# Optimization experiments

Hardware: AMD Instinct MI355X
Metric: run time of the kernel (lower is better)

Reference implementation:

```python
import jax, jax.numpy as jnp
import numpy as np

WL, FL = 64, 40
SCALE = 2.0 ** FL
CLIP_MAX = 2.0 ** (WL - FL - 1) - 2.0 ** (-FL)  # (2^(wl-1)-1)/2^fl
CLIP_MIN = -(2.0 ** (WL - FL - 1))
EPS = 1e-5
H = 8  # num_heads


def quant(x):
    # Fixed-point nearest-rounding quantizer: wl=64, fl=40.
    return jnp.clip(jnp.round(x * SCALE) / SCALE, CLIP_MIN, CLIP_MAX)


def setup_inputs() -> dict:
    key = jax.random.key(0)
    ks = jax.random.split(key, 9)
    N, S, C = 4096, 31, 512  # S = num_particles + 1 = 31 (hard-coded in module)
    SS = S * S
    return {
        "x": jax.random.normal(ks[0], (N, S, C), dtype=jnp.float32),
        "norm_gamma": jnp.ones((C,), jnp.float32),
        "norm_beta": jnp.zeros((C,), jnp.float32),
        "wq": jax.random.normal(ks[1], (C, C), jnp.float32) * 0.02,
        "wk": jax.random.normal(ks[2], (C, C), jnp.float32) * 0.02,
        "wv": jax.random.normal(ks[3], (C, C), jnp.float32) * 0.02,
        "wo": jax.random.normal(ks[4], (C, C), jnp.float32) * 0.02,
        "bo": jnp.zeros((C,), jnp.float32),
        "pre_gamma": jnp.ones((SS,), jnp.float32),
        "pre_beta": jnp.zeros((SS,), jnp.float32),
    }


def reference(x, norm_gamma, norm_beta, wq, wk, wv, wo, bo, pre_gamma, pre_beta):
    N, S, C = x.shape
    # BatchNorm1d(C) on x.transpose(1,2): per-channel stats over (batch, seq), training-mode (batch stats)
    mu = jnp.mean(x, axis=(0, 1))
    var = jnp.var(x, axis=(0, 1))
    out = quant((x - mu) * jax.lax.rsqrt(var + EPS) * norm_gamma + norm_beta)

    out_q = quant(out @ wq.T)
    out_k = quant(out @ wk.T)
    out_v = quant(out @ wv.T)

    q_ = out_q.reshape(N, S, H, C // H)
    k_ = out_k.reshape(N, S, H, C // H)
    v_ = out_v.reshape(N, S, H, C // H)

    energy = quant(jnp.einsum('nqhc,nkhc->nhqk', q_, k_))  # [N,H,S,S]

    # pre_exp_norm: BatchNorm1d(S*S) over reshaped energies; channel dim = S*S, stats over (batch, heads)
    e = energy.reshape(N, H, S * S)
    em = jnp.mean(e, axis=(0, 1))
    ev = jnp.var(e, axis=(0, 1))
    en = quant((e - em) * jax.lax.rsqrt(ev + EPS) * pre_gamma + pre_beta)
    energy_post = en.reshape(N, H, S, S)

    attention = quant(jax.nn.softmax(energy_post / jnp.sqrt(jnp.float32(C)), axis=-1))

    out = quant(jnp.einsum('nhql,nlhc->nqhc', attention, v_)).reshape(N, S, C)
    out = quant(out @ wo.T + bo)
    return quant(out + x)
```

## Files before the change

### kernel.cpp

```cpp
#include <hip/hip_runtime.h>
#include <cstdint>
#include <cstddef>

#define N_ 4096
#define S_ 31
#define C_ 512
#define H_ 8
#define M_ (N_*S_)
#define NH_ (N_*H_)

typedef unsigned short u16;
typedef unsigned char  u8;
typedef __bf16 v8bf __attribute__((ext_vector_type(8)));
typedef float  v4f  __attribute__((ext_vector_type(4)));
typedef float  v2f  __attribute__((ext_vector_type(2)));
typedef unsigned short v8u __attribute__((ext_vector_type(8)));

#define WS_STATS 2097152
#define WS_Q (WS_STATS + 32768)
#define WS_K (WS_Q + 67108864)
#define WS_V (WS_K + 67108864)

#define SCALE_QK 16.0f
#define SCALE_V  16.0f

__device__ __forceinline__ u16 f2bf(float f) {
  union { float f; unsigned u; } v; v.f = f;
  unsigned r = v.u + 0x7FFFu + ((v.u >> 16) & 1u);
  return (u16)(r >> 16);
}
__device__ __forceinline__ float bf2f(u16 v) {
  union { unsigned u; float f; } w; w.u = ((unsigned)v) << 16; return w.f;
}
__device__ __forceinline__ u8 enc1(float f) {
  return (u8)(__builtin_amdgcn_cvt_pk_fp8_f32(f, f, 0, false) & 0xff);
}
__device__ __forceinline__ unsigned enc4(float a, float b, float c, float d) {
  int w = __builtin_amdgcn_cvt_pk_fp8_f32(a, b, 0, false);
  w = __builtin_amdgcn_cvt_pk_fp8_f32(c, d, w, true);
  return (unsigned)w;
}
__device__ __forceinline__ v8bf dec8(uint2 u) {
  v2f p0 = __builtin_amdgcn_cvt_pk_f32_fp8((int)u.x, false);
  v2f p1 = __builtin_amdgcn_cvt_pk_f32_fp8((int)u.x, true);
  v2f p2 = __builtin_amdgcn_cvt_pk_f32_fp8((int)u.y, false);
  v2f p3 = __builtin_amdgcn_cvt_pk_f32_fp8((int)u.y, true);
  v8bf r;
  r[0]=(__bf16)p0[0]; r[1]=(__bf16)p0[1]; r[2]=(__bf16)p1[0]; r[3]=(__bf16)p1[1];
  r[4]=(__bf16)p2[0]; r[5]=(__bf16)p2[1]; r[6]=(__bf16)p3[0]; r[7]=(__bf16)p3[1];
  return r;
}

__global__ void k_init(const float* wq, const float* wk, const float* wv, const float* wo,
                       u16* wbf, float* statsf) {
  int gid = blockIdx.x * 256 + threadIdx.x;
  if (gid < 6144) statsf[gid] = 0.0f;
  int m = gid >> 18, o = gid & 262143;
  int e    = o & 7;
  int lane = (o >> 3) & 63;
  int kk   = (o >> 9) & 15;
  int j16  = o >> 13;
  int j = j16 * 16 + (lane & 15);
  int k = kk * 32 + (lane >> 4) * 8 + e;
  const float* src = (m == 0) ? wq : (m == 1) ? wk : (m == 2) ? wv : wo;
  wbf[(size_t)m * 262144 + o] = f2bf(src[j * 512 + k]);
}

__global__ void __launch_bounds__(512) k_xstats(const float* __restrict__ x, float* statsf) {
  int t = threadIdx.x;
  int c4 = (t & 127) * 4;
  int r0 = blockIdx.x * 512 + (t >> 7) * 128;
  float4 s = {0,0,0,0}, sq = {0,0,0,0};
  const float* p = x + (size_t)r0 * C_ + c4;
  for (int i = 0; i < 128; ++i) {
    float4 v = *(const float4*)(p + (size_t)i * C_);
    s.x += v.x; s.y += v.y; s.z += v.z; s.w += v.w;
    sq.x += v.x*v.x; sq.y += v.y*v.y; sq.z += v.z*v.z; sq.w += v.w*v.w;
  }
  atomicAdd(&statsf[c4+0], s.x); atomicAdd(&statsf[c4+1], s.y);
  atomicAdd(&statsf[c4+2], s.z); atomicAdd(&statsf[c4+3], s.w);
  atomicAdd(&statsf[512+c4+0], sq.x); atomicAdd(&statsf[512+c4+1], sq.y);
  atomicAdd(&statsf[512+c4+2], sq.z); atomicAdd(&statsf[512+c4+3], sq.w);
}

__global__ void k_finalize_ch(const float* gamma, const float* beta, float* statsf) {
  int c = threadIdx.x;
  float mu  = statsf[c] * (1.0f / (float)M_);
  float var = statsf[512 + c] * (1.0f / (float)M_) - mu * mu;
  float sc  = rsqrtf(var + 1e-5f) * gamma[c];
  statsf[1024 + c] = sc;
  statsf[1536 + c] = beta[c] - mu * sc;
}

__global__ void __launch_bounds__(512, 4)
k_qkv(const float* __restrict__ x, const u16* __restrict__ wbf,
      const float* __restrict__ statsf, u8* __restrict__ qg, u8* __restrict__ kg,
      u8* __restrict__ vt) {
  __shared__ float s_scale[C_], s_shift[C_];
  __shared__ u16 s_a[16*4*64*8];
  int t = threadIdx.x, nblk = blockIdx.x;
  int wave = t >> 6, lane = t & 63, l15 = lane & 15, quad = lane >> 4;
  s_scale[t] = statsf[1024+t]; s_shift[t] = statsf[1536+t];
  __syncthreads();

  const float* xb = x + (size_t)nblk * 2 * S_ * C_;
  for (int it = 0; it < 8; ++it) {
    int idx = t + it * 512;
    int row = idx >> 6, c8 = (idx & 63) << 3;
    int nl = row >> 5, s = row & 31;
    int kk = c8 >> 5, q4 = (c8 >> 3) & 3, mt = row >> 4, r15 = row & 15;
    u16* dst = s_a + ((((kk*4 + mt) << 6) | ((q4*16 + r15) ^ (kk & 7))) << 3);
    v8u o;
    if (s == 31) { o = (v8u){0,0,0,0,0,0,0,0}; }
    else {
      const float* g = xb + (size_t)(nl * 31 + s) * C_ + c8;
      float4 a = *(const float4*)g, b = *(const float4*)(g + 4);
      o[0]=f2bf(a.x*s_scale[c8+0]+s_shift[c8+0]); o[1]=f2bf(a.y*s_scale[c8+1]+s_shift[c8+1]);
      o[2]=f2bf(a.z*s_scale[c8+2]+s_shift[c8+2]); o[3]=f2bf(a.w*s_scale[c8+3]+s_shift[c8+3]);
      o[4]=f2bf(b.x*s_scale[c8+4]+s_shift[c8+4]); o[5]=f2bf(b.y*s_scale[c8+5]+s_shift[c8+5]);
      o[6]=f2bf(b.z*s_scale[c8+6]+s_shift[c8+6]); o[7]=f2bf(b.w*s_scale[c8+7]+s_shift[c8+7]);
    }
    *(v8u*)dst = o;
  }
  __syncthreads();

  #pragma unroll 1
  for (int ci = 0; ci < 3; ++ci) {
    const u16* B0 = wbf + (size_t)ci * 262144 + (size_t)wave * 32768 + (size_t)lane * 8;
    v4f acc[4][4];
    #pragma unroll
    for (int m = 0; m < 4; ++m)
      #pragma unroll
      for (int c = 0; c < 4; ++c) acc[m][c] = (v4f){0,0,0,0};

    #pragma unroll 2
    for (int kk = 0; kk < 16; ++kk) {
      v8bf a[4], b[4];
      #pragma unroll
      for (int m = 0; m < 4; ++m)
        a[m] = *(const v8bf*)(s_a + ((((kk*4 + m) << 6) | (lane ^ (kk & 7))) << 3));
      #pragma unroll
      for (int c = 0; c < 4; ++c)
        b[c] = *(const v8bf*)(B0 + (size_t)c * 8192 + kk * 512);
      #pragma unroll
      for (int m = 0; m < 4; ++m)
        #pragma unroll
        for (int c = 0; c < 4; ++c)
          acc[m][c] = __builtin_amdgcn_mfma_f32_16x16x32_bf16(a[m], b[c], acc[m][c], 0, 0, 0);
    }

    #pragma unroll
    for (int m = 0; m < 4; ++m) {
      int rbase = m*16 + quad*4;
      int nl = rbase >> 5, s0 = rbase & 31;
      size_t nbase = (size_t)(nblk*2 + nl) * 8;
      #pragma unroll
      for (int c = 0; c < 4; ++c) {
        int jj = wave*64 + c*16 + l15;
        int h = jj >> 6, d = jj & 63;
        if (ci == 2) {
          unsigned w = enc4(acc[m][c][0]*SCALE_V, acc[m][c][1]*SCALE_V,
                            acc[m][c][2]*SCALE_V, acc[m][c][3]*SCALE_V);
          *(unsigned*)(vt + ((nbase + h) * 2048) + d*32 + s0) = w;
        } else {
          u8* dst = ((ci == 0) ? qg : kg) + (nbase + h) * 2048 + (size_t)s0 * 64 + d;
          #pragma unroll
          for (int reg = 0; reg < 4; ++reg)
            dst[reg * 64] = enc1(acc[m][c][reg] * SCALE_QK);
        }
      }
    }
  }
}

__global__ void __launch_bounds__(512)
k_energy(u8* __restrict__ qg, const u8* __restrict__ kg) {
  int t = threadIdx.x;
  int wave = t >> 6, lane = t & 63, l15 = lane & 15, quad = lane >> 4;
  size_t nh = (size_t)blockIdx.x * 8 + wave;
  const u8* qp = qg + nh * 2048;
  const u8* kp = kg + nh * 2048;
  v8bf A[2][2], B[2][2];
  #pragma unroll
  for (int mt = 0; mt < 2; ++mt)
    #pragma unroll
    for (int kk = 0; kk < 2; ++kk) {
      A[mt][kk] = dec8(*(const uint2*)(qp + (mt*16 + l15)*64 + kk*32 + quad*8));
      B[mt][kk] = dec8(*(const uint2*)(kp + (mt*16 + l15)*64 + kk*32 + quad*8));
    }
  v4f acc[2][2];
  #pragma unroll
  for (int qt = 0; qt < 2; ++qt)
    #pragma unroll
    for (int kt = 0; kt < 2; ++kt) {
      v4f a = {0,0,0,0};
      a = __builtin_amdgcn_mfma_f32_16x16x32_bf16(A[qt][0], B[kt][0], a, 0, 0, 0);
      a = __builtin_amdgcn_mfma_f32_16x16x32_bf16(A[qt][1], B[kt][1], a, 0, 0, 0);
      acc[qt][kt] = a;
    }
  u16* ep = (u16*)(qg + nh * 2048);
  const float inv = 1.0f / (SCALE_QK * SCALE_QK);
  #pragma unroll
  for (int qt = 0; qt < 2; ++qt)
    #pragma unroll
    for (int kt = 0; kt < 2; ++kt) {
      int k = kt*16 + l15;
      #pragma unroll
      for (int reg = 0; reg < 4; ++reg) {
        int q = qt*16 + quad*4 + reg;
        ep[q*32 + k] = f2bf(acc[qt][kt][reg] * inv);
      }
    }
}

__global__ void __launch_bounds__(256) k_estats(const u16* __restrict__ eg, float* statsf) {
  int t = threadIdx.x;
  int r0 = blockIdx.x * 128;
  float s[4] = {0,0,0,0}, sq[4] = {0,0,0,0};
  for (int i = 0; i < 128; ++i) {
    uint2 u = *(const uint2*)(eg + (size_t)(r0 + i) * 1024 + t * 4);
    float v0 = bf2f((u16)(u.x & 0xffff)), v1 = bf2f((u16)(u.x >> 16));
    float v2 = bf2f((u16)(u.y & 0xffff)), v3 = bf2f((u16)(u.y >> 16));
    s[0]+=v0; s[1]+=v1; s[2]+=v2; s[3]+=v3;
    sq[0]+=v0*v0; sq[1]+=v1*v1; sq[2]+=v2*v2; sq[3]+=v3*v3;
  }
  #pragma unroll
  for (int j = 0; j < 4; ++j) {
    atomicAdd(&statsf[2048 + t*4 + j], s[j]);
    atomicAdd(&statsf[3072 + t*4 + j], sq[j]);
  }
}

__global__ void k_finalize_e(const float* pg, const float* pb, float* statsf) {
  int c = threadIdx.x;
  int q = c >> 5, k = c & 31;
  const float invC = 0.04419417382415922f;
  float s2 = 0.f, sh2 = 0.f;
  if (q < 31 && k < 31) {
    int ss = q*31 + k;
    float mu  = statsf[2048 + c] * (1.0f / (float)NH_);
    float var = statsf[3072 + c] * (1.0f / (float)NH_) - mu * mu;
    float sc  = rsqrtf(var + 1e-5f) * pg[ss];
    s2  = sc * invC;
    sh2 = (pb[ss] - mu * sc) * invC;
  }
  statsf[4096 + c] = s2;
  statsf[5120 + c] = sh2;
}

__global__ void __launch_bounds__(512, 4)
k_oproj(const float* __restrict__ x, const u16* __restrict__ wbf,
        const float* __restrict__ statsf, const u16* __restrict__ eg,
        const u8* __restrict__ vt, const float* __restrict__ bo, float* __restrict__ out) {
  __shared__ u16 s_a[16*4*64*8];
  __shared__ u16 s_attn[8][1024];
  int t = threadIdx.x, nblk = blockIdx.x;
  int wave = t >> 6, lane = t & 63, l15 = lane & 15, quad = lane >> 4;

  int q = lane & 31, half = lane >> 5;
  #pragma unroll 1
  for (int tk = 0; tk < 2; ++tk) {
    int task = wave * 2 + tk;
    int nl = task >> 3, h = task & 7;
    size_t nh = (size_t)(nblk*2 + nl) * 8 + h;
    const u16* ep = eg + nh * 1024;
    int cb = q*32 + half*16;
    v8u e0 = *(const v8u*)(ep + cb);
    v8u e1 = *(const v8u*)(ep + cb + 8);
    const float* s2g  = statsf + 4096 + cb;
    const float* sh2g = statsf + 5120 + cb;
    float lg[16];
    #pragma unroll
    for (int j = 0; j < 8; ++j) lg[j]   = bf2f(e0[j]) * s2g[j]   + sh2g[j];
    #pragma unroll
    for (int j = 0; j < 8; ++j) lg[8+j] = bf2f(e1[j]) * s2g[8+j] + sh2g[8+j];
    if (half) lg[15] = -1e30f;
    float mx = lg[0];
    #pragma unroll
    for (int j = 1; j < 16; ++j) mx = fmaxf(mx, lg[j]);
    mx = fmaxf(mx, __shfl_xor(mx, 32));
    float sum = 0.f;
    #pragma unroll
    for (int j = 0; j < 16; ++j) { lg[j] = __expf(lg[j] - mx); sum += lg[j]; }
    sum += __shfl_xor(sum, 32);
    float r = (q == 31) ? 0.f : (1.0f / sum);
    v8u o0, o1;
    #pragma unroll
    for (int j = 0; j < 8; ++j) { o0[j] = f2bf(lg[j] * r); o1[j] = f2bf(lg[8+j] * r); }
    *(v8u*)(&s_attn[wave][cb]) = o0;
    *(v8u*)(&s_attn[wave][cb + 8]) = o1;
    v8bf a0 = *(const v8bf*)(&s_attn[wave][(l15)*32 + quad*8]);
    v8bf a1 = *(const v8bf*)(&s_attn[wave][(16 + l15)*32 + quad*8]);
    const float invV = 1.0f / SCALE_V;
    #pragma unroll
    for (int ct = 0; ct < 4; ++ct) {
      uint2 u = *(const uint2*)(vt + nh*2048 + (ct*16 + l15)*32 + quad*8);
      v8bf b = dec8(u);
      v4f c0 = {0,0,0,0}, c1 = {0,0,0,0};
      c0 = __builtin_amdgcn_mfma_f32_16x16x32_bf16(a0, b, c0, 0, 0, 0);
      c1 = __builtin_amdgcn_mfma_f32_16x16x32_bf16(a1, b, c1, 0, 0, 0);
      int ch = h*64 + ct*16 + l15;
      int kkA = ch >> 5, qA = (ch >> 3) & 3, pA = ch & 7;
      #pragma unroll
      for (int reg = 0; reg < 4; ++reg) {
        int rm = quad*4 + reg;
        s_a[((((kkA*4 + nl*2 + 0) << 6) | (qA*16 + rm)) << 3) + pA] = f2bf(c0[reg] * invV);
        s_a[((((kkA*4 + nl*2 + 1) << 6) | (qA*16 + rm)) << 3) + pA] = f2bf(c1[reg] * invV);
      }
    }
  }
  __syncthreads();

  {
    const u16* B0 = wbf + (size_t)3 * 262144 + (size_t)wave * 32768 + (size_t)lane * 8;
    v4f acc[4][4];
    #pragma unroll
    for (int m = 0; m < 4; ++m)
      #pragma unroll
      for (int c = 0; c < 4; ++c) acc[m][c] = (v4f){0,0,0,0};
    #pragma unroll 2
    for (int kk = 0; kk < 16; ++kk) {
      v8bf a[4], b[4];
      #pragma unroll
      for (int m = 0; m < 4; ++m)
        a[m] = *(const v8bf*)(s_a + ((((kk*4 + m) << 6) | lane) << 3));
      #pragma unroll
      for (int c = 0; c < 4; ++c)
        b[c] = *(const v8bf*)(B0 + (size_t)c * 8192 + kk * 512);
      #pragma unroll
      for (int m = 0; m < 4; ++m)
        #pragma unroll
        for (int c = 0; c < 4; ++c)
          acc[m][c] = __builtin_amdgcn_mfma_f32_16x16x32_bf16(a[m], b[c], acc[m][c], 0, 0, 0);
    }
    #pragma unroll
    for (int m = 0; m < 4; ++m) {
      int rbase = m*16 + quad*4;
      int nl = rbase >> 5, s0 = rbase & 31;
      #pragma unroll
      for (int c = 0; c < 4; ++c) {
        int j = wave*64 + c*16 + l15;
        float bj = bo[j];
        #pragma unroll
        for (int reg = 0; reg < 4; ++reg) {
          int s = s0 + reg;
          if (s < 31) {
            size_t off = (size_t)((nblk*2 + nl) * 31 + s) * C_ + j;
            out[off] = acc[m][c][reg] + bj + x[off];
          }
        }
      }
    }
  }
}

extern "C" void kernel_launch(void* const* d_in, const int* in_sizes, int n_in,
                              void* d_out, int out_size, void* d_ws, size_t ws_size,
                              hipStream_t stream) {
  const float* x     = (const float*)d_in[0];
  const float* gamma = (const float*)d_in[1];
  const float* beta  = (const float*)d_in[2];
  const float* wq    = (const float*)d_in[3];
  const float* wk    = (const float*)d_in[4];
  const float* wv    = (const float*)d_in[5];
  const float* wo    = (const float*)d_in[6];
  const float* bo    = (const float*)d_in[7];
  const float* pg    = (const float*)d_in[8];
  const float* pb    = (const float*)d_in[9];

  char* ws = (char*)d_ws;
  u16*   wbf    = (u16*)ws;
  float* statsf = (float*)(ws + WS_STATS);
  u8*    qg     = (u8*)(ws + WS_Q);
  u8*    kg     = (u8*)(ws + WS_K);
  u8*    vtp    = (u8*)(ws + WS_V);
  float* outp   = (float*)d_out;

  k_init<<<4096, 256, 0, stream>>>(wq, wk, wv, wo, wbf, statsf);
  k_xstats<<<248, 512, 0, stream>>>(x, statsf);
  k_finalize_ch<<<1, 512, 0, stream>>>(gamma, beta, statsf);
  k_qkv<<<2048, 512, 0, stream>>>(x, wbf, statsf, qg, kg, vtp);
  k_energy<<<4096, 512, 0, stream>>>(qg, kg);
  k_estats<<<256, 256, 0, stream>>>((const u16*)qg, statsf);
  k_finalize_e<<<1, 1024, 0, stream>>>(pg, pb, statsf);
  k_oproj<<<2048, 512, 0, stream>>>(x, wbf, statsf, (const u16*)qg, vtp, bo, outp);
}
```

Baseline: 1.016 ms.

## Fuse QK energy computation into QKV projection kernel via LDS staging

The QK^T energy computation is folded into the QKV projection kernel. Each wave stages its fp8 Q and K head tiles in swizzled LDS and runs the energy MFMAs directly, writing bf16 energies. This removes the k_energy launch and the global write and read-back of Q and K (128MB of fp8 traffic). In exchange it raises register pressure from holding the packed Q and K results, adds byte-wise LDS stores, and lengthens the fused kernel.

```diff
diff --git a/kernel.cpp b/kernel.cpp
--- a/kernel.cpp
+++ b/kernel.cpp
@@ -31,9 +31,6 @@
 }
 __device__ __forceinline__ float bf2f(u16 v) {
   union { unsigned u; float f; } w; w.u = ((unsigned)v) << 16; return w.f;
-}
-__device__ __forceinline__ u8 enc1(float f) {
-  return (u8)(__builtin_amdgcn_cvt_pk_fp8_f32(f, f, 0, false) & 0xff);
 }
 __device__ __forceinline__ unsigned enc4(float a, float b, float c, float d) {
   int w = __builtin_amdgcn_cvt_pk_fp8_f32(a, b, 0, false);
@@ -92,10 +89,31 @@
   statsf[1536 + c] = beta[c] - mu * sc;
 }
 
+__device__ __forceinline__ void gemm64(const u16* sa, const u16* B0, v4f (&acc)[4][4], int lane) {
+  #pragma unroll
+  for (int m = 0; m < 4; ++m)
+    #pragma unroll
+    for (int c = 0; c < 4; ++c) acc[m][c] = (v4f){0,0,0,0};
+  #pragma unroll 2
+  for (int kk = 0; kk < 16; ++kk) {
+    v8bf a[4], b[4];
+    #pragma unroll
+    for (int m = 0; m < 4; ++m)
+      a[m] = *(const v8bf*)(sa + ((((kk*4 + m) << 6) | (lane ^ (kk & 7))) << 3));
+    #pragma unroll
+    for (int c = 0; c < 4; ++c)
+      b[c] = *(const v8bf*)(B0 + (size_t)c * 8192 + kk * 512);
+    #pragma unroll
+    for (int m = 0; m < 4; ++m)
+      #pragma unroll
+      for (int c = 0; c < 4; ++c)
+        acc[m][c] = __builtin_amdgcn_mfma_f32_16x16x32_bf16(a[m], b[c], acc[m][c], 0, 0, 0);
+  }
+}
+
 __global__ void __launch_bounds__(512, 4)
 k_qkv(const float* __restrict__ x, const u16* __restrict__ wbf,
-      const float* __restrict__ statsf, u8* __restrict__ qg, u8* __restrict__ kg,
-      u8* __restrict__ vt) {
+      const float* __restrict__ statsf, u8* __restrict__ eg8, u8* __restrict__ vt) {
   __shared__ float s_scale[C_], s_shift[C_];
   __shared__ u16 s_a[16*4*64*8];
   int t = threadIdx.x, nblk = blockIdx.x;
@@ -124,93 +142,87 @@
   }
   __syncthreads();
 
+  v4f acc[4][4];
+
+  gemm64(s_a, wbf + (size_t)2 * 262144 + (size_t)wave * 32768 + (size_t)lane * 8, acc, lane);
+  #pragma unroll
+  for (int m = 0; m < 4; ++m) {
+    int rbase = m*16 + quad*4;
+    int nl = rbase >> 5, s0 = rbase & 31;
+    size_t nbase = (size_t)(nblk*2 + nl) * 8;
+    #pragma unroll
+    for (int c = 0; c < 4; ++c) {
+      int d = c*16 + l15;
+      unsigned w = enc4(acc[m][c][0]*SCALE_V, acc[m][c][1]*SCALE_V,
+                        acc[m][c][2]*SCALE_V, acc[m][c][3]*SCALE_V);
+      *(unsigned*)(vt + ((nbase + wave) * 2048) + d*32 + s0) = w;
+    }
+  }
+
+  unsigned qpack[16];
+  gemm64(s_a, wbf + (size_t)0 * 262144 + (size_t)wave * 32768 + (size_t)lane * 8, acc, lane);
+  #pragma unroll
+  for (int m = 0; m < 4; ++m)
+    #pragma unroll
+    for (int c = 0; c < 4; ++c)
+      qpack[m*4+c] = enc4(acc[m][c][0]*SCALE_QK, acc[m][c][1]*SCALE_QK,
+                          acc[m][c][2]*SCALE_QK, acc[m][c][3]*SCALE_QK);
+
+  unsigned kpack[16];
+  gemm64(s_a, wbf + (size_t)1 * 262144 + (size_t)wave * 32768 + (size_t)lane * 8, acc, lane);
+  #pragma unroll
+  for (int m = 0; m < 4; ++m)
+    #pragma unroll
+    for (int c = 0; c < 4; ++c)
+      kpack[m*4+c] = enc4(acc[m][c][0]*SCALE_QK, acc[m][c][1]*SCALE_QK,
+                          acc[m][c][2]*SCALE_QK, acc[m][c][3]*SCALE_QK);
+
+  __syncthreads();
+
+  u8* scr = (u8*)s_a + wave * 8192;
+  #pragma unroll
+  for (int m = 0; m < 4; ++m)
+    #pragma unroll
+    for (int c = 0; c < 4; ++c) {
+      int d = c*16 + l15;
+      #pragma unroll
+      for (int reg = 0; reg < 4; ++reg) {
+        int r = m*16 + quad*4 + reg;
+        int dd = d ^ ((r & 7) << 3);
+        scr[r*64 + dd]        = (u8)(qpack[m*4+c] >> (reg*8));
+        scr[4096 + r*64 + dd] = (u8)(kpack[m*4+c] >> (reg*8));
+      }
+    }
+
+  const float inv = 1.0f / (SCALE_QK * SCALE_QK);
   #pragma unroll 1
-  for (int ci = 0; ci < 3; ++ci) {
-    const u16* B0 = wbf + (size_t)ci * 262144 + (size_t)wave * 32768 + (size_t)lane * 8;
-    v4f acc[4][4];
-    #pragma unroll
-    for (int m = 0; m < 4; ++m)
-      #pragma unroll
-      for (int c = 0; c < 4; ++c) acc[m][c] = (v4f){0,0,0,0};
-
-    #pragma unroll 2
-    for (int kk = 0; kk < 16; ++kk) {
-      v8bf a[4], b[4];
-      #pragma unroll
-      for (int m = 0; m < 4; ++m)
-        a[m] = *(const v8bf*)(s_a + ((((kk*4 + m) << 6) | (lane ^ (kk & 7))) << 3));
-      #pragma unroll
-      for (int c = 0; c < 4; ++c)
-        b[c] = *(const v8bf*)(B0 + (size_t)c * 8192 + kk * 512);
-      #pragma unroll
-      for (int m = 0; m < 4; ++m)
+  for (int n = 0; n < 2; ++n) {
+    v8bf A[2][2], B[2][2];
+    #pragma unroll
+    for (int mt = 0; mt < 2; ++mt)
+      #pragma unroll
+      for (int kk = 0; kk < 2; ++kk) {
+        int r = n*32 + mt*16 + l15;
+        int dA = (kk*32 + quad*8) ^ ((r & 7) << 3);
+        A[mt][kk] = dec8(*(const uint2*)(scr + r*64 + dA));
+        B[mt][kk] = dec8(*(const uint2*)(scr + 4096 + r*64 + dA));
+      }
+    u16* ep = (u16*)(eg8 + (((size_t)(nblk*2 + n) * 8 + wave) * 2048));
+    #pragma unroll
+    for (int qt = 0; qt < 2; ++qt)
+      #pragma unroll
+      for (int kt = 0; kt < 2; ++kt) {
+        v4f a2 = {0,0,0,0};
+        a2 = __builtin_amdgcn_mfma_f32_16x16x32_bf16(A[qt][0], B[kt][0], a2, 0, 0, 0);
+        a2 = __builtin_amdgcn_mfma_f32_16x16x32_bf16(A[qt][1], B[kt][1], a2, 0, 0, 0);
+        int k = kt*16 + l15;
         #pragma unroll
-        for (int c = 0; c < 4; ++c)
-          acc[m][c] = __builtin_amdgcn_mfma_f32_16x16x32_bf16(a[m], b[c], acc[m][c], 0, 0, 0);
-    }
-
-    #pragma unroll
-    for (int m = 0; m < 4; ++m) {
-      int rbase = m*16 + quad*4;
-      int nl = rbase >> 5, s0 = rbase & 31;
-      size_t nbase = (size_t)(nblk*2 + nl) * 8;
-      #pragma unroll
-      for (int c = 0; c < 4; ++c) {
-        int jj = wave*64 + c*16 + l15;
-        int h = jj >> 6, d = jj & 63;
-        if (ci == 2) {
-          unsigned w = enc4(acc[m][c][0]*SCALE_V, acc[m][c][1]*SCALE_V,
-                            acc[m][c][2]*SCALE_V, acc[m][c][3]*SCALE_V);
-          *(unsigned*)(vt + ((nbase + h) * 2048) + d*32 + s0) = w;
-        } else {
-          u8* dst = ((ci == 0) ? qg : kg) + (nbase + h) * 2048 + (size_t)s0 * 64 + d;
-          #pragma unroll
-          for (int reg = 0; reg < 4; ++reg)
-            dst[reg * 64] = enc1(acc[m][c][reg] * SCALE_QK);
+        for (int reg = 0; reg < 4; ++reg) {
+          int q = qt*16 + quad*4 + reg;
+          ep[q*32 + k] = f2bf(a2[reg] * inv);
         }
       }
-    }
-  }
-}
-
-__global__ void __launch_bounds__(512)
-k_energy(u8* __restrict__ qg, const u8* __restrict__ kg) {
-  int t = threadIdx.x;
-  int wave = t >> 6, lane = t & 63, l15 = lane & 15, quad = lane >> 4;
-  size_t nh = (size_t)blockIdx.x * 8 + wave;
-  const u8* qp = qg + nh * 2048;
-  const u8* kp = kg + nh * 2048;
-  v8bf A[2][2], B[2][2];
-  #pragma unroll
-  for (int mt = 0; mt < 2; ++mt)
-    #pragma unroll
-    for (int kk = 0; kk < 2; ++kk) {
-      A[mt][kk] = dec8(*(const uint2*)(qp + (mt*16 + l15)*64 + kk*32 + quad*8));
-      B[mt][kk] = dec8(*(const uint2*)(kp + (mt*16 + l15)*64 + kk*32 + quad*8));
-    }
-  v4f acc[2][2];
-  #pragma unroll
-  for (int qt = 0; qt < 2; ++qt)
-    #pragma unroll
-    for (int kt = 0; kt < 2; ++kt) {
-      v4f a = {0,0,0,0};
-      a = __builtin_amdgcn_mfma_f32_16x16x32_bf16(A[qt][0], B[kt][0], a, 0, 0, 0);
-      a = __builtin_amdgcn_mfma_f32_16x16x32_bf16(A[qt][1], B[kt][1], a, 0, 0, 0);
-      acc[qt][kt] = a;
-    }
-  u16* ep = (u16*)(qg + nh * 2048);
-  const float inv = 1.0f / (SCALE_QK * SCALE_QK);
-  #pragma unroll
-  for (int qt = 0; qt < 2; ++qt)
-    #pragma unroll
-    for (int kt = 0; kt < 2; ++kt) {
-      int k = kt*16 + l15;
-      #pragma unroll
-      for (int reg = 0; reg < 4; ++reg) {
-        int q = qt*16 + quad*4 + reg;
-        ep[q*32 + k] = f2bf(acc[qt][kt][reg] * inv);
-      }
-    }
+  }
 }
 
 __global__ void __launch_bounds__(256) k_estats(const u16* __restrict__ eg, float* statsf) {
@@ -371,17 +383,15 @@
   char* ws = (char*)d_ws;
   u16*   wbf    = (u16*)ws;
   float* statsf = (float*)(ws + WS_STATS);
-  u8*    qg     = (u8*)(ws + WS_Q);
-  u8*    kg     = (u8*)(ws + WS_K);
+  u8*    eg8    = (u8*)(ws + WS_Q);
   u8*    vtp    = (u8*)(ws + WS_V);
   float* outp   = (float*)d_out;
 
   k_init<<<4096, 256, 0, stream>>>(wq, wk, wv, wo, wbf, statsf);
   k_xstats<<<248, 512, 0, stream>>>(x, statsf);
   k_finalize_ch<<<1, 512, 0, stream>>>(gamma, beta, statsf);
-  k_qkv<<<2048, 512, 0, stream>>>(x, wbf, statsf, qg, kg, vtp);
-  k_energy<<<4096, 512, 0, stream>>>(qg, kg);
-  k_estats<<<256, 256, 0, stream>>>((const u16*)qg, statsf);
+  k_qkv<<<2048, 512, 0, stream>>>(x, wbf, statsf, eg8, vtp);
+  k_estats<<<256, 256, 0, stream>>>((const u16*)eg8, statsf);
   k_finalize_e<<<1, 1024, 0, stream>>>(pg, pb, statsf);
-  k_oproj<<<2048, 512, 0, stream>>>(x, wbf, statsf, (const u16*)qg, vtp, bo, outp);
-}
+  k_oproj<<<2048, 512, 0, stream>>>(x, wbf, statsf, (const u16*)eg8, vtp, bo, outp);
+}
```

After: 986.2 us, median of 2. -2.9%, faster.
